# Optimization experiments

Hardware: AMD Instinct MI355X
Metric: run time of the kernel (lower is better)

The kernel has to match this reference:

```python
import jax, jax.numpy as jnp
import numpy as np

B, S, D, HID, H, VOCAB, DFF = 4, 2048, 512, 512, 8, 32000, 2048
DK = HID // H   # per-head Q/K dim
DV = D // H     # per-head V dim


def sinusoidal_pe(L, d):
    pos = jnp.arange(L, dtype=jnp.float32)[:, None]
    i = jnp.arange(d, dtype=jnp.float32)[None, :]
    ang = pos / jnp.power(jnp.float32(10000.0), i / d)
    return jnp.where(jnp.arange(d)[None, :] % 2 == 0, jnp.sin(ang), jnp.cos(ang))  # [L, d]


def layer_norm(x, gamma, beta, eps=1e-5):
    mu = jnp.mean(x, axis=-1, keepdims=True)
    var = jnp.mean((x - mu) ** 2, axis=-1, keepdims=True)
    return (x - mu) * jax.lax.rsqrt(var + eps) * gamma + beta


def setup_inputs() -> dict:
    key = jax.random.key(0)
    ks = jax.random.split(key, 24)
    n = lambda k, shape, fan: jax.random.normal(k, shape, dtype=jnp.float32) / np.sqrt(fan)
    inp = {
        'x': jax.random.randint(ks[0], (B, S), 0, VOCAB),
        'emb': n(ks[1], (VOCAB, D), D),
        'WfQ': n(ks[2], (D, HID), D), 'bfQ': jnp.zeros((HID,), jnp.float32),
        'WfK': n(ks[3], (D, HID), D), 'bfK': jnp.zeros((HID,), jnp.float32),
        'WfV': n(ks[4], (D, D), D),   'bfV': jnp.zeros((D,), jnp.float32),
        'WQ': n(ks[5], (H, HID, DK), HID), 'bQ': jnp.zeros((H, DK), jnp.float32),
        'WK': n(ks[6], (H, HID, DK), HID), 'bK': jnp.zeros((H, DK), jnp.float32),
        'WV': n(ks[7], (H, D, DV), D),     'bV': jnp.zeros((H, DV), jnp.float32),
        'Wo': n(ks[8], (D, D), D),   'bo': jnp.zeros((D,), jnp.float32),
        'W1': n(ks[9], (D, DFF), D), 'b1': jnp.zeros((DFF,), jnp.float32),
        'W2': n(ks[10], (DFF, D), DFF), 'b2': jnp.zeros((D,), jnp.float32),
        'gamma': jnp.ones((D,), jnp.float32), 'beta': jnp.zeros((D,), jnp.float32),
    }
    return inp


def reference(x, emb, WfQ, bfQ, WfK, bfK, WfV, bfV, WQ, bQ, WK, bK, WV, bV,
              Wo, bo, W1, b1, W2, b2, gamma, beta):
    z = emb[x] + sinusoidal_pe(x.shape[1], D)[None]            # [B,S,D]
    Q = z @ WfQ + bfQ                                           # [B,S,HID]
    K = z @ WfK + bfK
    V = z @ WfV + bfV                                           # [B,S,D]
    # per-head projections (batched equivalent of the per-head Linear loop)
    Qh = jnp.einsum('bsd,hdk->bhsk', Q, WQ) + bQ[None, :, None, :]  # [B,H,S,DK]
    Kh = jnp.einsum('bsd,hdk->bhsk', K, WK) + bK[None, :, None, :]
    Vh = jnp.einsum('bsd,hdv->bhsv', V, WV) + bV[None, :, None, :]  # [B,H,S,DV]
    scores = jnp.einsum('bhqk,bhsk->bhqs', Qh, Kh) / np.sqrt(DK)    # [B,H,S,S]
    attn = jax.nn.softmax(scores, axis=-1)
    heads = jnp.einsum('bhqs,bhsv->bhqv', attn, Vh)                 # [B,H,S,DV]
    concat = heads.transpose(0, 2, 1, 3).reshape(x.shape[0], x.shape[1], D)
    attn_out = concat @ Wo + bo
    a = layer_norm(attn_out + z, gamma, beta)
    ffn = jax.nn.relu(a @ W1 + b1) @ W2 + b2
    out = layer_norm(ffn + a, gamma, beta)   # same (shared) LayerNorm params, as in source
    return jax.nn.relu(out)
```

## Files before the change

### kernel.cpp

```cpp
#include <hip/hip_runtime.h>
#include <math.h>

typedef __bf16 bf16;
typedef __bf16 bf16x8 __attribute__((ext_vector_type(8)));
typedef __bf16 bf16x4 __attribute__((ext_vector_type(4)));
typedef _Float16 f16;
typedef _Float16 f16x8 __attribute__((ext_vector_type(8)));
typedef _Float16 f16x4 __attribute__((ext_vector_type(4)));
typedef _Float16 f16x2 __attribute__((ext_vector_type(2)));
typedef __fp16 h16x2 __attribute__((ext_vector_type(2)));
typedef float f32x4 __attribute__((ext_vector_type(4)));
typedef unsigned int u32;

#define S_LEN 2048
#define QSCALE 0.18033688011112042f

#if __has_builtin(__builtin_amdgcn_exp2f)
#define EXP2(x) __builtin_amdgcn_exp2f(x)
#else
#define EXP2(x) exp2f(x)
#endif

__device__ __forceinline__ void gload_lds16(const void* g, void* l) {
  __builtin_amdgcn_global_load_lds((const __attribute__((address_space(1))) u32*)g,
                                   (__attribute__((address_space(3))) u32*)l, 16, 0, 0);
}

__global__ __launch_bounds__(256) void embed_pe(const int* __restrict__ x,
    const float* __restrict__ emb, bf16* __restrict__ zb)
{
  const int row = blockIdx.x;
  const int s = row & (S_LEN - 1);
  const int tok = x[row];
  const float* e = emb + (size_t)tok * 512;
  bf16* zbr = zb + (size_t)row * 512;
  for (int i = threadIdx.x; i < 512; i += 256) {
    float invf = __expf((float)i * (-9.210340371976184f / 512.0f));
    float ang = (float)s * invf;
    float pe = (i & 1) ? __cosf(ang) : __sinf(ang);
    zbr[i] = (bf16)(e[i] + pe);
  }
}

__global__ __launch_bounds__(256) void conv_t(
    const float* __restrict__ Wo, const float* __restrict__ W1, const float* __restrict__ W2,
    const float* __restrict__ WQ, const float* __restrict__ WK, const float* __restrict__ WV,
    const float* __restrict__ WfQ, const float* __restrict__ WfK, const float* __restrict__ WfV,
    bf16* __restrict__ wot, bf16* __restrict__ w1t, bf16* __restrict__ w2t,
    bf16* __restrict__ wqt, bf16* __restrict__ wkt, bf16* __restrict__ wvt,
    bf16* __restrict__ wfqp, bf16* __restrict__ wfkp, bf16* __restrict__ wfvp)
{
  __shared__ float T[64][65];
  const int y = blockIdx.y, x = blockIdx.x;
  if (y >= 6) {
    int g = x * 256 + threadIdx.x;
    const float* in = y == 6 ? WfQ : (y == 7 ? WfK : WfV);
    bf16* outp = y == 6 ? wfqp : (y == 7 ? wfkp : wfvp);
    float4 v = *(const float4*)(in + (size_t)g * 4);
    bf16x4 o = {(bf16)v.x, (bf16)v.y, (bf16)v.z, (bf16)v.w};
    *(bf16x4*)(outp + (size_t)g * 4) = o;
    return;
  }
  const int tx = threadIdx.x & 63, ty = threadIdx.x >> 6;
  const float* src; bf16* dst;
  int src_cols, dst_cols; float scale = 1.f;
  if (y == 0) {
    if (x >= 64) return;
    int kt = x & 7, nt = x >> 3;
    src = Wo + (size_t)(kt * 64) * 512 + nt * 64; src_cols = 512;
    dst = wot + (size_t)(nt * 64) * 512 + kt * 64; dst_cols = 512;
  } else if (y == 1) {
    int kt = x & 7, nt = x >> 3;
    src = W1 + (size_t)(kt * 64) * 2048 + nt * 64; src_cols = 2048;
    dst = w1t + (size_t)(nt * 64) * 512 + kt * 64; dst_cols = 512;
  } else if (y == 2) {
    int kt = x & 31, nt = x >> 5;
    src = W2 + (size_t)(kt * 64) * 512 + nt * 64; src_cols = 512;
    dst = w2t + (size_t)(nt * 64) * 2048 + kt * 64; dst_cols = 2048;
  } else {
    if (x >= 64) return;
    const float* W = y == 3 ? WQ : (y == 4 ? WK : WV);
    bf16* o = y == 3 ? wqt : (y == 4 ? wkt : wvt);
    if (y == 3) scale = QSCALE;
    int h = x >> 3, rt = x & 7;
    src = W + (size_t)(h * 512 + rt * 64) * 64; src_cols = 64;
    dst = o + (size_t)(h * 64) * 512 + rt * 64; dst_cols = 512;
  }
  #pragma unroll
  for (int i = 0; i < 16; i++) {
    int rr = i * 4 + ty;
    T[rr][tx] = src[(size_t)rr * src_cols + tx];
  }
  __syncthreads();
  #pragma unroll
  for (int i = 0; i < 16; i++) {
    int rr = i * 4 + ty;
    dst[(size_t)rr * dst_cols + tx] = (bf16)(T[tx][rr] * scale);
  }
}

__global__ __launch_bounds__(256) void bias_comb(
    const float* __restrict__ bfQ, const float* __restrict__ bfK, const float* __restrict__ bfV,
    const float* __restrict__ WQ, const float* __restrict__ WK, const float* __restrict__ WV,
    const float* __restrict__ bQ, const float* __restrict__ bK, const float* __restrict__ bV,
    float* __restrict__ bc)
{
  int n = blockIdx.x * 4 + (threadIdx.x >> 6);
  int lane = threadIdx.x & 63;
  int z = n >> 9, hk = n & 511, h = hk >> 6, k = hk & 63;
  const float* bf = z == 0 ? bfQ : (z == 1 ? bfK : bfV);
  const float* W  = z == 0 ? WQ  : (z == 1 ? WK  : WV);
  const float* bH = z == 0 ? bQ  : (z == 1 ? bK  : bV);
  float s = 0.f;
  for (int e = lane; e < 512; e += 64)
    s += bf[e] * W[((size_t)h * 512 + e) * 64 + k];
  #pragma unroll
  for (int m = 1; m < 64; m <<= 1) s += __shfl_xor(s, m, 64);
  if (lane == 0) {
    float v = s + bH[h * 64 + k];
    if (z == 0) v *= QSCALE;
    bc[n] = v;
  }
}

__global__ __launch_bounds__(256) void gemm_comb(
    const bf16* __restrict__ wqt, const bf16* __restrict__ wkt, const bf16* __restrict__ wvt,
    const bf16* __restrict__ wfqp, const bf16* __restrict__ wfkp, const bf16* __restrict__ wfvp,
    bf16* __restrict__ wc)
{
  __shared__ bf16 As[128 * 32];
  __shared__ bf16 Bs[64 * 32];
  const int z = blockIdx.z;
  const bf16* A  = z == 0 ? wqt : (z == 1 ? wkt : wvt);
  const bf16* Bt = z == 0 ? wfqp : (z == 1 ? wfkp : wfvp);
  bf16* outb = wc + (size_t)z * 262144;
  const int tid = threadIdx.x;
  const int wave = tid >> 6, lane = tid & 63, quad = lane >> 4, l16 = lane & 15;
  const int row0 = blockIdx.x * 128, col0 = blockIdx.y * 64;
  const int wm = wave >> 1, wn = wave & 1;
  f32x4 acc[4][2] = {};

  for (int kk = 0; kk < 512; kk += 32) {
    __syncthreads();
    #pragma unroll
    for (int r = 0; r < 2; r++) {
      int c = r * 256 + tid;
      gload_lds16(A + (size_t)(row0 + (c >> 2)) * 512 + kk + (c & 3) * 8, As + c * 8);
    }
    gload_lds16(Bt + (size_t)(col0 + (tid >> 2)) * 512 + kk + (tid & 3) * 8, Bs + tid * 8);
    __syncthreads();
    bf16x8 af[4], bfr[2];
    #pragma unroll
    for (int i = 0; i < 4; i++)
      af[i] = *(const bf16x8*)(As + (wm * 64 + i * 16 + l16) * 32 + quad * 8);
    #pragma unroll
    for (int i = 0; i < 2; i++)
      bfr[i] = *(const bf16x8*)(Bs + (wn * 32 + i * 16 + l16) * 32 + quad * 8);
    #pragma unroll
    for (int mt = 0; mt < 4; mt++)
      #pragma unroll
      for (int nt = 0; nt < 2; nt++)
        acc[mt][nt] = __builtin_amdgcn_mfma_f32_16x16x32_bf16(af[mt], bfr[nt], acc[mt][nt], 0, 0, 0);
  }
  #pragma unroll
  for (int nt = 0; nt < 2; nt++) {
    int col = col0 + wn * 32 + nt * 16 + l16;
    #pragma unroll
    for (int mt = 0; mt < 4; mt++) {
      int rowb = row0 + wm * 64 + mt * 16 + quad * 4;
      #pragma unroll
      for (int i = 0; i < 4; i++)
        outb[(size_t)(rowb + i) * 512 + col] = (bf16)acc[mt][nt][i];
    }
  }
}

#define GEMM_CORE(A_, Bt_, K_, KK0_, ITERS_)                                            \
  bf16x8 ar0, ar1, br0, br1;                                                            \
  const int c0 = tid, c1 = 256 + tid;                                                   \
  const size_t aoff0 = (size_t)(row0 + (c0 >> 2)) * (K_) + (c0 & 3) * 8;                \
  const size_t aoff1 = (size_t)(row0 + (c1 >> 2)) * (K_) + (c1 & 3) * 8;                \
  const size_t boff0 = (size_t)(col0 + (c0 >> 2)) * (K_) + (c0 & 3) * 8;                \
  const size_t boff1 = (size_t)(col0 + (c1 >> 2)) * (K_) + (c1 & 3) * 8;                \
  ar0 = *(const bf16x8*)((A_) + aoff0 + (KK0_));                                        \
  ar1 = *(const bf16x8*)((A_) + aoff1 + (KK0_));                                        \
  br0 = *(const bf16x8*)((Bt_) + boff0 + (KK0_));                                       \
  br1 = *(const bf16x8*)((Bt_) + boff1 + (KK0_));                                       \
  for (int it = 0; it < (ITERS_); it++) {                                               \
    bf16* AsB = As[it & 1];                                                             \
    bf16* BsB = Bs[it & 1];                                                             \
    *(bf16x8*)(AsB + c0 * 8) = ar0;                                                     \
    *(bf16x8*)(AsB + c1 * 8) = ar1;                                                     \
    *(bf16x8*)(BsB + c0 * 8) = br0;                                                     \
    *(bf16x8*)(BsB + c1 * 8) = br1;                                                     \
    __syncthreads();                                                                    \
    if (it + 1 < (ITERS_)) {                                                            \
      int kk = (KK0_) + (it + 1) * 32;                                                  \
      ar0 = *(const bf16x8*)((A_) + aoff0 + kk);                                        \
      ar1 = *(const bf16x8*)((A_) + aoff1 + kk);                                        \
      br0 = *(const bf16x8*)((Bt_) + boff0 + kk);                                      \
      br1 = *(const bf16x8*)((Bt_) + boff1 + kk);                                      \
    }                                                                                   \
    bf16x8 af[4], bfr[4];                                                               \
    _Pragma("unroll")                                                                   \
    for (int i = 0; i < 4; i++)                                                         \
      af[i] = *(const bf16x8*)(AsB + (wm * 64 + i * 16 + l16) * 32 + quad * 8);         \
    _Pragma("unroll")                                                                   \
    for (int i = 0; i < 4; i++)                                                         \
      bfr[i] = *(const bf16x8*)(BsB + (wn * 64 + i * 16 + l16) * 32 + quad * 8);        \
    _Pragma("unroll")                                                                   \
    for (int mt = 0; mt < 4; mt++)                                                      \
      _Pragma("unroll")                                                                 \
      for (int nt = 0; nt < 4; nt++)                                                    \
        acc[mt][nt] = __builtin_amdgcn_mfma_f32_16x16x32_bf16(af[mt], bfr[nt], acc[mt][nt], 0, 0, 0); \
  }

__global__ __launch_bounds__(256) void gemm_bt(
    const bf16* __restrict__ A, const bf16* __restrict__ Bt,
    const float* __restrict__ bias, bf16* __restrict__ outb,
    int M, int N, int K, int relu)
{
  __shared__ bf16 As[2][4096];
  __shared__ bf16 Bs[2][4096];
  const int tid = threadIdx.x;
  const int wave = tid >> 6, lane = tid & 63, quad = lane >> 4, l16 = lane & 15;
  const int row0 = blockIdx.x * 128, col0 = blockIdx.y * 128;
  const int wm = wave >> 1, wn = wave & 1;
  f32x4 acc[4][4] = {};
  GEMM_CORE(A, Bt, K, 0, K / 32)

  #pragma unroll
  for (int nt = 0; nt < 4; nt++) {
    int col = col0 + wn * 64 + nt * 16 + l16;
    float bv = bias[col];
    #pragma unroll
    for (int mt = 0; mt < 4; mt++) {
      int rowb = row0 + wm * 64 + mt * 16 + quad * 4;
      #pragma unroll
      for (int i = 0; i < 4; i++) {
        float v = acc[mt][nt][i] + bv;
        if (relu) v = fmaxf(v, 0.f);
        outb[(size_t)(rowb + i) * N + col] = (bf16)v;
      }
    }
  }
}

__global__ __launch_bounds__(256) void gemm_qkv(
    const bf16* __restrict__ A, const bf16* __restrict__ Bt,
    const float* __restrict__ bias, f16* __restrict__ qk, f16* __restrict__ Vt)
{
  __shared__ bf16 As[2][4096];
  __shared__ bf16 Bs[2][4096];
  const int tid = threadIdx.x;
  const int wave = tid >> 6, lane = tid & 63, quad = lane >> 4, l16 = lane & 15;
  const int row0 = blockIdx.x * 128, col0 = blockIdx.y * 128;
  const int wm = wave >> 1, wn = wave & 1;
  f32x4 acc[4][4] = {};
  GEMM_CORE(A, Bt, 512, 0, 16)

  #pragma unroll
  for (int nt = 0; nt < 4; nt++) {
    int col = col0 + wn * 64 + nt * 16 + l16;
    float bv = bias[col];
    if (col < 1024) {
      #pragma unroll
      for (int mt = 0; mt < 4; mt++) {
        int rowb = row0 + wm * 64 + mt * 16 + quad * 4;
        #pragma unroll
        for (int i = 0; i < 4; i++)
          qk[(size_t)(rowb + i) * 1024 + col] = (f16)(acc[mt][nt][i] + bv);
      }
    } else {
      int h = (col - 1024) >> 6, dv = col & 63;
      #pragma unroll
      for (int mt = 0; mt < 4; mt++) {
        int rowb = row0 + wm * 64 + mt * 16 + quad * 4;
        int b = rowb >> 11, s = rowb & 2047;
        f16x4 vv;
        #pragma unroll
        for (int i = 0; i < 4; i++) vv[i] = (f16)(acc[mt][nt][i] + bv);
        *(f16x4*)(Vt + ((size_t)((b * 8 + h) * 64 + dv)) * 2048 + s) = vv;
      }
    }
  }
}

__global__ __launch_bounds__(256) void gemm_part(
    const bf16* __restrict__ A, const bf16* __restrict__ Bt,
    bf16* __restrict__ Pa, bf16* __restrict__ Pb, int N, int K, int Kh)
{
  __shared__ bf16 As[2][4096];
  __shared__ bf16 Bs[2][4096];
  const int tid = threadIdx.x;
  const int wave = tid >> 6, lane = tid & 63, quad = lane >> 4, l16 = lane & 15;
  const int row0 = blockIdx.x * 128, col0 = blockIdx.y * 128;
  const int wm = wave >> 1, wn = wave & 1;
  const int kk0 = blockIdx.z * Kh;
  bf16* P = blockIdx.z ? Pb : Pa;
  f32x4 acc[4][4] = {};
  GEMM_CORE(A, Bt, K, kk0, Kh / 32)

  #pragma unroll
  for (int nt = 0; nt < 4; nt++) {
    int col = col0 + wn * 64 + nt * 16 + l16;
    #pragma unroll
    for (int mt = 0; mt < 4; mt++) {
      int rowb = row0 + wm * 64 + mt * 16 + quad * 4;
      #pragma unroll
      for (int i = 0; i < 4; i++)
        P[(size_t)(rowb + i) * N + col] = (bf16)acc[mt][nt][i];
    }
  }
}

__global__ __launch_bounds__(256) void flash_attn(
    const f16* __restrict__ qk, const f16* __restrict__ Vt,
    bf16* __restrict__ Op, float* __restrict__ Rp)
{
  __shared__ f16 Ks[2][4096];
  __shared__ f16 Vs[2][4096];
  const int bh = blockIdx.y, b = bh >> 3, h = bh & 7;
  const int q0 = blockIdx.x * 128;
  const int quarter = blockIdx.z;
  const int tid = threadIdx.x;
  const int wave = tid >> 6, lane = tid & 63, quad = lane >> 4, l16 = lane & 15;

  const f16* Qb = qk + ((size_t)b * S_LEN) * 1024 + h * 64;
  const f16* Kb = Qb + 512;
  const f16* Vtb = Vt + ((size_t)bh * 64) * 2048;
  const int key0 = quarter * 512;

  f16x8 qf[2][2];
  #pragma unroll
  for (int f = 0; f < 2; f++) {
    int qrow = q0 + wave * 32 + f * 16 + l16;
    #pragma unroll
    for (int kh = 0; kh < 2; kh++)
      qf[f][kh] = *(const f16x8*)(Qb + (size_t)qrow * 1024 + kh * 32 + quad * 8);
  }

  f32x4 O[2][4] = {};
  float rs[2] = {0.f, 0.f};
  const int swz = l16 & 7;

  f16x8 kreg[2], vreg[2];
  const int srow = tid >> 3, soff = tid & 7;
  const int srow1 = srow + 32;

  {
    int kb = key0;
    kreg[0] = *(const f16x8*)(Kb + (size_t)(kb + srow) * 1024 + soff * 8);
    vreg[0] = *(const f16x8*)(Vtb + (size_t)srow * 2048 + kb + soff * 8);
    kreg[1] = *(const f16x8*)(Kb + (size_t)(kb + srow1) * 1024 + soff * 8);
    vreg[1] = *(const f16x8*)(Vtb + (size_t)srow1 * 2048 + kb + soff * 8);
  }

  for (int c = 0; c < 8; c++) {
    f16* KsB = Ks[c & 1];
    f16* VsB = Vs[c & 1];
    *(f16x8*)(KsB + srow * 64 + ((soff ^ (srow & 7)) * 8)) = kreg[0];
    *(f16x8*)(VsB + srow * 64 + ((soff ^ (srow & 7)) * 8)) = vreg[0];
    *(f16x8*)(KsB + srow1 * 64 + ((soff ^ (srow1 & 7)) * 8)) = kreg[1];
    *(f16x8*)(VsB + srow1 * 64 + ((soff ^ (srow1 & 7)) * 8)) = vreg[1];
    __syncthreads();
    if (c < 7) {
      int kb = key0 + (c + 1) * 64;
      kreg[0] = *(const f16x8*)(Kb + (size_t)(kb + srow) * 1024 + soff * 8);
      vreg[0] = *(const f16x8*)(Vtb + (size_t)srow * 2048 + kb + soff * 8);
      kreg[1] = *(const f16x8*)(Kb + (size_t)(kb + srow1) * 1024 + soff * 8);
      vreg[1] = *(const f16x8*)(Vtb + (size_t)srow1 * 2048 + kb + soff * 8);
    }

    #pragma unroll
    for (int nt = 0; nt < 4; nt++) {
      const f16* kp = KsB + (nt * 16 + l16) * 64;
      f16x8 kf0 = *(const f16x8*)(kp + ((quad ^ swz) * 8));
      f16x8 kf1 = *(const f16x8*)(kp + (((4 + quad) ^ swz) * 8));
      f16x4 pf[2];
      #pragma unroll
      for (int f = 0; f < 2; f++) {
        f32x4 a = {};
        a = __builtin_amdgcn_mfma_f32_16x16x32_f16(kf0, qf[f][0], a, 0, 0, 0);
        a = __builtin_amdgcn_mfma_f32_16x16x32_f16(kf1, qf[f][1], a, 0, 0, 0);
        float e0 = EXP2(a[0]);
        float e1 = EXP2(a[1]);
        float e2 = EXP2(a[2]);
        float e3 = EXP2(a[3]);
        h16x2 lo = __builtin_amdgcn_cvt_pkrtz(e0, e1);
        h16x2 hi = __builtin_amdgcn_cvt_pkrtz(e2, e3);
        f16x2 lo2 = __builtin_bit_cast(f16x2, lo);
        f16x2 hi2 = __builtin_bit_cast(f16x2, hi);
        pf[f] = __builtin_shufflevector(lo2, hi2, 0, 1, 2, 3);
#if __has_builtin(__builtin_amdgcn_fdot2)
        const f16x2 ones2 = {(f16)1.f, (f16)1.f};
        rs[f] = __builtin_amdgcn_fdot2(lo2, ones2, rs[f], false);
        rs[f] = __builtin_amdgcn_fdot2(hi2, ones2, rs[f], false);
#else
        rs[f] += (e0 + e1) + (e2 + e3);
#endif
      }
      int vchunk = nt * 2 + (quad >> 1);
      #pragma unroll
      for (int mt = 0; mt < 4; mt++) {
        const f16* vp = VsB + (mt * 16 + l16) * 64 + ((vchunk ^ swz) * 8) + (quad & 1) * 4;
        f16x4 vf = *(const f16x4*)vp;
        #pragma unroll
        for (int f = 0; f < 2; f++)
          O[f][mt] = __builtin_amdgcn_mfma_f32_16x16x16f16(vf, pf[f], O[f][mt], 0, 0, 0);
      }
    }
  }

  #pragma unroll
  for (int f = 0; f < 2; f++) {
    rs[f] += __shfl_xor(rs[f], 16, 64);
    rs[f] += __shfl_xor(rs[f], 32, 64);
  }

  #pragma unroll
  for (int f = 0; f < 2; f++) {
    bf16* ob = (f == 0 ? (bf16*)&Ks[0][0] : (bf16*)&Vs[0][0]) + wave * 1024;
    #pragma unroll
    for (int mt = 0; mt < 4; mt++) {
      bf16x4 w;
      #pragma unroll
      for (int i = 0; i < 4; i++) w[i] = (bf16)O[f][mt][i];
      int chunk = mt * 2 + (quad >> 1);
      *(bf16x4*)(ob + l16 * 64 + ((chunk ^ (l16 & 7)) << 3) + (quad & 1) * 4) = w;
    }
  }
  asm volatile("s_waitcnt lgkmcnt(0)" ::: "memory");
  const size_t obase = (size_t)(quarter * 32 + bh) * 2048;
  #pragma unroll
  for (int f = 0; f < 2; f++) {
    const bf16* ob = (f == 0 ? (const bf16*)&Ks[0][0] : (const bf16*)&Vs[0][0]) + wave * 1024;
    int row = lane >> 2, cc = (lane & 3) * 2;
    bf16x8 o0 = *(const bf16x8*)(ob + row * 64 + ((cc ^ (row & 7)) << 3));
    bf16x8 o1 = *(const bf16x8*)(ob + row * 64 + (((cc + 1) ^ (row & 7)) << 3));
    size_t g = (obase + q0 + wave * 32 + f * 16 + row) * 64 + (lane & 3) * 16;
    *(bf16x8*)(Op + g) = o0;
    *(bf16x8*)(Op + g + 8) = o1;
    if (quad == f)
      Rp[obase + q0 + wave * 32 + f * 16 + l16] = rs[f];
  }
}

__global__ __launch_bounds__(256) void attn_merge(const bf16* __restrict__ Op,
    const float* __restrict__ Rp, bf16* __restrict__ concat)
{
  int t = blockIdx.x * 256 + threadIdx.x;
  int dv4 = t & 15, s = (t >> 4) & 2047, bh = t >> 15;
  int rb = bh * 2048 + s;
  float r = (Rp[rb] + Rp[65536 + rb]) + (Rp[131072 + rb] + Rp[196608 + rb]);
  float inv = 1.f / r;
  size_t ia = ((size_t)bh * 2048 + s) * 64 + dv4 * 4;
  bf16x4 p0 = *(const bf16x4*)(Op + ia);
  bf16x4 p1 = *(const bf16x4*)(Op + 4194304ull + ia);
  bf16x4 p2 = *(const bf16x4*)(Op + 8388608ull + ia);
  bf16x4 p3 = *(const bf16x4*)(Op + 12582912ull + ia);
  bf16x4 o;
  #pragma unroll
  for (int i = 0; i < 4; i++)
    o[i] = (bf16)((((float)p0[i] + (float)p1[i]) + ((float)p2[i] + (float)p3[i])) * inv);
  int b = bh >> 3, h = bh & 7;
  *(bf16x4*)(concat + ((size_t)(b * 2048 + s)) * 512 + h * 64 + dv4 * 4) = o;
}

__global__ __launch_bounds__(256) void ln_merge(const bf16* __restrict__ Pa,
    const bf16* __restrict__ Pb, const float* __restrict__ badd,
    const bf16* __restrict__ resid, const float* __restrict__ gamma,
    const float* __restrict__ beta, float* __restrict__ outf,
    bf16* __restrict__ outb, int relu)
{
  const int row = blockIdx.x * 4 + (threadIdx.x >> 6);
  const int lane = threadIdx.x & 63;
  const size_t base = (size_t)row * 512;
  const int e0 = lane * 8;
  bf16x8 pa = *(const bf16x8*)(Pa + base + e0);
  bf16x8 pb = *(const bf16x8*)(Pb + base + e0);
  bf16x8 rr = *(const bf16x8*)(resid + base + e0);
  float4 C0 = *(const float4*)(badd + e0);
  float4 C1 = *(const float4*)(badd + e0 + 4);
  float v[8];
  v[0] = (float)pa[0] + (float)pb[0] + (float)rr[0] + C0.x;
  v[1] = (float)pa[1] + (float)pb[1] + (float)rr[1] + C0.y;
  v[2] = (float)pa[2] + (float)pb[2] + (float)rr[2] + C0.z;
  v[3] = (float)pa[3] + (float)pb[3] + (float)rr[3] + C0.w;
  v[4] = (float)pa[4] + (float)pb[4] + (float)rr[4] + C1.x;
  v[5] = (float)pa[5] + (float)pb[5] + (float)rr[5] + C1.y;
  v[6] = (float)pa[6] + (float)pb[6] + (float)rr[6] + C1.z;
  v[7] = (float)pa[7] + (float)pb[7] + (float)rr[7] + C1.w;
  float s = 0.f;
  #pragma unroll
  for (int i = 0; i < 8; i++) s += v[i];
  #pragma unroll
  for (int m = 1; m < 64; m <<= 1) s += __shfl_xor(s, m, 64);
  float mu = s * (1.f / 512.f);
  float d[8], q = 0.f;
  #pragma unroll
  for (int i = 0; i < 8; i++) { d[i] = v[i] - mu; q += d[i] * d[i]; }
  #pragma unroll
  for (int m = 1; m < 64; m <<= 1) q += __shfl_xor(q, m, 64);
  float rsn = rsqrtf(q * (1.f / 512.f) + 1e-5f);
  float4 g0 = *(const float4*)(gamma + e0);
  float4 g1 = *(const float4*)(gamma + e0 + 4);
  float4 b0 = *(const float4*)(beta + e0);
  float4 b1 = *(const float4*)(beta + e0 + 4);
  float y[8];
  y[0] = d[0] * rsn * g0.x + b0.x; y[1] = d[1] * rsn * g0.y + b0.y;
  y[2] = d[2] * rsn * g0.z + b0.z; y[3] = d[3] * rsn * g0.w + b0.w;
  y[4] = d[4] * rsn * g1.x + b1.x; y[5] = d[5] * rsn * g1.y + b1.y;
  y[6] = d[6] * rsn * g1.z + b1.z; y[7] = d[7] * rsn * g1.w + b1.w;
  if (relu) {
    #pragma unroll
    for (int i = 0; i < 8; i++) y[i] = fmaxf(y[i], 0.f);
  }
  if (outf) {
    float4 o0 = {y[0], y[1], y[2], y[3]}, o1 = {y[4], y[5], y[6], y[7]};
    *(float4*)(outf + base + e0) = o0;
    *(float4*)(outf + base + e0 + 4) = o1;
  }
  if (outb) {
    bf16x8 ob;
    #pragma unroll
    for (int i = 0; i < 8; i++) ob[i] = (bf16)y[i];
    *(bf16x8*)(outb + base + e0) = ob;
  }
}

extern "C" void kernel_launch(void* const* d_in, const int* in_sizes, int n_in,
                              void* d_out, int out_size, void* d_ws, size_t ws_size,
                              hipStream_t stream)
{
  const int*   x    = (const int*)  d_in[0];
  const float* emb  = (const float*)d_in[1];
  const float* WfQ  = (const float*)d_in[2];
  const float* bfQv = (const float*)d_in[3];
  const float* WfK  = (const float*)d_in[4];
  const float* bfKv = (const float*)d_in[5];
  const float* WfV  = (const float*)d_in[6];
  const float* bfVv = (const float*)d_in[7];
  const float* WQ   = (const float*)d_in[8];
  const float* bQ   = (const float*)d_in[9];
  const float* WK   = (const float*)d_in[10];
  const float* bK   = (const float*)d_in[11];
  const float* WV   = (const float*)d_in[12];
  const float* bV   = (const float*)d_in[13];
  const float* Wo   = (const float*)d_in[14];
  const float* bo   = (const float*)d_in[15];
  const float* W1   = (const float*)d_in[16];
  const float* b1   = (const float*)d_in[17];
  const float* W2   = (const float*)d_in[18];
  const float* b2   = (const float*)d_in[19];
  const float* gamma= (const float*)d_in[20];
  const float* beta = (const float*)d_in[21];
  float* out = (float*)d_out;

  char* ws = (char*)d_ws;
  const size_t MB = 1024ull * 1024;
  bf16*  bz   = (bf16*) (ws);
  f16*   qkh  = (f16*)  (ws + 8 * MB);
  f16*   Vt   = (f16*)  (ws + 24 * MB);
  bf16*  Op   = (bf16*) (ws + 32 * MB);
  float* Rp   = (float*)(ws + 64 * MB);
  bf16*  concat = (bf16*)(ws + 66 * MB);
  bf16*  PaW  = (bf16*) (ws + 32 * MB);
  bf16*  PbW  = (bf16*) (ws + 40 * MB);
  bf16*  ffn1 = (bf16*) (ws + 8 * MB);
  bf16*  Pa2  = (bf16*) (ws + 40 * MB);
  bf16*  Pb2  = (bf16*) (ws + 48 * MB);
  char* wp = ws + 74 * MB;
  bf16* wfqp = (bf16*)(wp);
  bf16* wfkp = (bf16*)(wp + 512 * 1024);
  bf16* wfvp = (bf16*)(wp + 1024 * 1024);
  bf16* wqt  = (bf16*)(wp + 1536 * 1024);
  bf16* wkt  = (bf16*)(wp + 2048 * 1024);
  bf16* wvt  = (bf16*)(wp + 2560 * 1024);
  bf16* wc   = (bf16*)(wp + 3072 * 1024);
  bf16* wot  = (bf16*)(wp + 4608 * 1024);
  bf16* w1t  = (bf16*)(wp + 5120 * 1024);
  bf16* w2t  = (bf16*)(wp + 7168 * 1024);
  float* bc  = (float*)(wp + 9216 * 1024);

  conv_t<<<dim3(256, 9), 256, 0, stream>>>(Wo, W1, W2, WQ, WK, WV, WfQ, WfK, WfV,
                                           wot, w1t, w2t, wqt, wkt, wvt, wfqp, wfkp, wfvp);
  bias_comb<<<384, 256, 0, stream>>>(bfQv, bfKv, bfVv, WQ, WK, WV, bQ, bK, bV, bc);
  gemm_comb<<<dim3(4, 8, 3), 256, 0, stream>>>(wqt, wkt, wvt, wfqp, wfkp, wfvp, wc);

  embed_pe<<<8192, 256, 0, stream>>>(x, emb, bz);

  gemm_qkv<<<dim3(64, 12), 256, 0, stream>>>(bz, wc, bc, qkh, Vt);
  flash_attn<<<dim3(16, 32, 4), 256, 0, stream>>>(qkh, Vt, Op, Rp);
  attn_merge<<<4096, 256, 0, stream>>>(Op, Rp, concat);

  gemm_part<<<dim3(64, 4, 2), 256, 0, stream>>>(concat, wot, PaW, PbW, 512, 512, 256);
  ln_merge<<<2048, 256, 0, stream>>>(PaW, PbW, bo, bz, gamma, beta, nullptr, bz, 0);
  gemm_bt<<<dim3(64, 16), 256, 0, stream>>>(bz, w1t, b1, ffn1, 8192, 2048, 512, 1);
  gemm_part<<<dim3(64, 4, 2), 256, 0, stream>>>(ffn1, w2t, Pa2, Pb2, 512, 2048, 1024);
  ln_merge<<<2048, 256, 0, stream>>>(Pa2, Pb2, b2, bz, gamma, beta, out, nullptr, 1);
}
```

Baseline: 325.7 us.

## Load GEMM tiles via direct global-to-LDS and compute softmax row sums with MFMA

```diff
diff --git a/kernel.cpp b/kernel.cpp
--- a/kernel.cpp
+++ b/kernel.cpp
@@ -176,38 +176,26 @@
 }
 
 #define GEMM_CORE(A_, Bt_, K_, KK0_, ITERS_)                                            \
-  bf16x8 ar0, ar1, br0, br1;                                                            \
   const int c0 = tid, c1 = 256 + tid;                                                   \
   const size_t aoff0 = (size_t)(row0 + (c0 >> 2)) * (K_) + (c0 & 3) * 8;                \
   const size_t aoff1 = (size_t)(row0 + (c1 >> 2)) * (K_) + (c1 & 3) * 8;                \
   const size_t boff0 = (size_t)(col0 + (c0 >> 2)) * (K_) + (c0 & 3) * 8;                \
   const size_t boff1 = (size_t)(col0 + (c1 >> 2)) * (K_) + (c1 & 3) * 8;                \
-  ar0 = *(const bf16x8*)((A_) + aoff0 + (KK0_));                                        \
-  ar1 = *(const bf16x8*)((A_) + aoff1 + (KK0_));                                        \
-  br0 = *(const bf16x8*)((Bt_) + boff0 + (KK0_));                                       \
-  br1 = *(const bf16x8*)((Bt_) + boff1 + (KK0_));                                       \
   for (int it = 0; it < (ITERS_); it++) {                                               \
-    bf16* AsB = As[it & 1];                                                             \
-    bf16* BsB = Bs[it & 1];                                                             \
-    *(bf16x8*)(AsB + c0 * 8) = ar0;                                                     \
-    *(bf16x8*)(AsB + c1 * 8) = ar1;                                                     \
-    *(bf16x8*)(BsB + c0 * 8) = br0;                                                     \
-    *(bf16x8*)(BsB + c1 * 8) = br1;                                                     \
+    const int kk = (KK0_) + it * 32;                                                    \
     __syncthreads();                                                                    \
-    if (it + 1 < (ITERS_)) {                                                            \
-      int kk = (KK0_) + (it + 1) * 32;                                                  \
-      ar0 = *(const bf16x8*)((A_) + aoff0 + kk);                                        \
-      ar1 = *(const bf16x8*)((A_) + aoff1 + kk);                                        \
-      br0 = *(const bf16x8*)((Bt_) + boff0 + kk);                                      \
-      br1 = *(const bf16x8*)((Bt_) + boff1 + kk);                                      \
-    }                                                                                   \
+    gload_lds16((A_) + aoff0 + kk, As + c0 * 8);                                        \
+    gload_lds16((A_) + aoff1 + kk, As + c1 * 8);                                        \
+    gload_lds16((Bt_) + boff0 + kk, Bs + c0 * 8);                                       \
+    gload_lds16((Bt_) + boff1 + kk, Bs + c1 * 8);                                       \
+    __syncthreads();                                                                    \
     bf16x8 af[4], bfr[4];                                                               \
     _Pragma("unroll")                                                                   \
     for (int i = 0; i < 4; i++)                                                         \
-      af[i] = *(const bf16x8*)(AsB + (wm * 64 + i * 16 + l16) * 32 + quad * 8);         \
+      af[i] = *(const bf16x8*)(As + (wm * 64 + i * 16 + l16) * 32 + quad * 8);          \
     _Pragma("unroll")                                                                   \
     for (int i = 0; i < 4; i++)                                                         \
-      bfr[i] = *(const bf16x8*)(BsB + (wn * 64 + i * 16 + l16) * 32 + quad * 8);        \
+      bfr[i] = *(const bf16x8*)(Bs + (wn * 64 + i * 16 + l16) * 32 + quad * 8);         \
     _Pragma("unroll")                                                                   \
     for (int mt = 0; mt < 4; mt++)                                                      \
       _Pragma("unroll")                                                                 \
@@ -220,8 +208,8 @@
     const float* __restrict__ bias, bf16* __restrict__ outb,
     int M, int N, int K, int relu)
 {
-  __shared__ bf16 As[2][4096];
-  __shared__ bf16 Bs[2][4096];
+  __shared__ bf16 As[4096];
+  __shared__ bf16 Bs[4096];
   const int tid = threadIdx.x;
   const int wave = tid >> 6, lane = tid & 63, quad = lane >> 4, l16 = lane & 15;
   const int row0 = blockIdx.x * 128, col0 = blockIdx.y * 128;
@@ -250,8 +238,8 @@
     const bf16* __restrict__ A, const bf16* __restrict__ Bt,
     const float* __restrict__ bias, f16* __restrict__ qk, f16* __restrict__ Vt)
 {
-  __shared__ bf16 As[2][4096];
-  __shared__ bf16 Bs[2][4096];
+  __shared__ bf16 As[4096];
+  __shared__ bf16 Bs[4096];
   const int tid = threadIdx.x;
   const int wave = tid >> 6, lane = tid & 63, quad = lane >> 4, l16 = lane & 15;
   const int row0 = blockIdx.x * 128, col0 = blockIdx.y * 128;
@@ -290,8 +278,8 @@
     const bf16* __restrict__ A, const bf16* __restrict__ Bt,
     bf16* __restrict__ Pa, bf16* __restrict__ Pb, int N, int K, int Kh)
 {
-  __shared__ bf16 As[2][4096];
-  __shared__ bf16 Bs[2][4096];
+  __shared__ bf16 As[4096];
+  __shared__ bf16 Bs[4096];
   const int tid = threadIdx.x;
   const int wave = tid >> 6, lane = tid & 63, quad = lane >> 4, l16 = lane & 15;
   const int row0 = blockIdx.x * 128, col0 = blockIdx.y * 128;
@@ -341,7 +329,8 @@
   }
 
   f32x4 O[2][4] = {};
-  float rs[2] = {0.f, 0.f};
+  f32x4 Osum[2] = {};
+  const f16x4 onesA = {(f16)1.f, (f16)1.f, (f16)1.f, (f16)1.f};
   const int swz = l16 & 7;
 
   f16x8 kreg[2], vreg[2];
@@ -392,13 +381,7 @@
         f16x2 lo2 = __builtin_bit_cast(f16x2, lo);
         f16x2 hi2 = __builtin_bit_cast(f16x2, hi);
         pf[f] = __builtin_shufflevector(lo2, hi2, 0, 1, 2, 3);
-#if __has_builtin(__builtin_amdgcn_fdot2)
-        const f16x2 ones2 = {(f16)1.f, (f16)1.f};
-        rs[f] = __builtin_amdgcn_fdot2(lo2, ones2, rs[f], false);
-        rs[f] = __builtin_amdgcn_fdot2(hi2, ones2, rs[f], false);
-#else
-        rs[f] += (e0 + e1) + (e2 + e3);
-#endif
+        Osum[f] = __builtin_amdgcn_mfma_f32_16x16x16f16(onesA, pf[f], Osum[f], 0, 0, 0);
       }
       int vchunk = nt * 2 + (quad >> 1);
       #pragma unroll
@@ -410,12 +393,6 @@
           O[f][mt] = __builtin_amdgcn_mfma_f32_16x16x16f16(vf, pf[f], O[f][mt], 0, 0, 0);
       }
     }
-  }
-
-  #pragma unroll
-  for (int f = 0; f < 2; f++) {
-    rs[f] += __shfl_xor(rs[f], 16, 64);
-    rs[f] += __shfl_xor(rs[f], 32, 64);
   }
 
   #pragma unroll
@@ -442,7 +419,7 @@
     *(bf16x8*)(Op + g) = o0;
     *(bf16x8*)(Op + g + 8) = o1;
     if (quad == f)
-      Rp[obase + q0 + wave * 32 + f * 16 + l16] = rs[f];
+      Rp[obase + q0 + wave * 32 + f * 16 + l16] = Osum[f][0];
   }
 }
 
```

New measurement: 333.6 us. +2.4%, slower.
